# Kernel tuning notes

Measured on AMD Instinct MI355X. Metric: run time of the kernel, lower is better.

Reference implementation:

```python
import jax, jax.numpy as jnp
import numpy as np

B, NELEC, NATOMS, SH_PER_ATOM, NORB, NCTR = 512, 100, 20, 30, 300, 2
NBAS = NATOMS * SH_PER_ATOM  # 600 == NORB * NCTR


def _ipow(x, k):
    # x**k for integer k in {0,1,2}; safe for negative x (cartesian harmonics)
    return jnp.where(k == 0, jnp.ones_like(x), jnp.where(k == 1, x, x * x))


def setup_inputs() -> dict:
    key = jax.random.key(0)
    ks = jax.random.split(key, 7)
    pos = jax.random.normal(ks[0], (B, NELEC * 3), jnp.float32)
    atom_coords = jax.random.normal(ks[1], (NATOMS, 3), jnp.float32)
    bas_exp = jax.random.uniform(ks[2], (NBAS,), jnp.float32, 0.5, 3.0)
    bas_n = jax.random.randint(ks[3], (NBAS,), 0, 3).astype(jnp.float32)
    norm_cst = jax.random.uniform(ks[4], (NBAS,), jnp.float32, 0.5, 1.5)
    bas_coeffs = jax.random.normal(ks[5], (NBAS,), jnp.float32)
    bas_kxyz = jax.random.randint(ks[6], (NBAS, 3), 0, 3)  # kx, ky, kz exponents
    index_ctr = jnp.repeat(jnp.arange(NORB, dtype=jnp.int32), NCTR)  # nbas -> norb
    return {"pos": pos, "atom_coords": atom_coords, "bas_exp": bas_exp,
            "bas_n": bas_n, "norm_cst": norm_cst, "bas_coeffs": bas_coeffs,
            "bas_kxyz": bas_kxyz, "index_ctr": index_ctr}


def reference(pos, atom_coords, bas_exp, bas_n, norm_cst, bas_coeffs, bas_kxyz, index_ctr):
    # gather: per-shell atom coordinates  (NBAS, 3)
    bas_coords = jnp.repeat(atom_coords, SH_PER_ATOM, axis=0)
    # electron - basis-center displacement  (B, Nelec, NBAS, 3)
    xyz = pos.reshape(-1, NELEC, 1, 3) - bas_coords[None, None]
    r2 = jnp.sum(xyz * xyz, axis=-1)                 # (B, Nelec, NBAS)
    r = jnp.sqrt(r2)
    # radial_gaussian: r^n * exp(-alpha r^2)
    R = jnp.power(r, bas_n) * jnp.exp(-bas_exp * r2)
    # cartesian harmonics: x^kx * y^ky * z^kz
    Y = (_ipow(xyz[..., 0], bas_kxyz[:, 0]) *
         _ipow(xyz[..., 1], bas_kxyz[:, 1]) *
         _ipow(xyz[..., 2], bas_kxyz[:, 2]))
    # ao kernel + contraction (segment-sum over basis fns into orbitals)
    vals = (norm_cst * bas_coeffs) * R * Y           # (B, Nelec, NBAS)
    ao = jnp.zeros((pos.shape[0], NELEC, NORB), vals.dtype).at[:, :, index_ctr].add(vals)
    return ao
```

## Files before the change

### kernel.cpp

```cpp
#include <hip/hip_runtime.h>

#define BATCH   512
#define NELEC   100
#define NATOMS  20
#define SH      30
#define NORB    300
#define NBAS    600
#define NROWS   (BATCH * NELEC)
#define GROWS   16
#define NGRP    2
#define ROWS    (GROWS * NGRP)
#define NBLOCKS (NROWS / ROWS)
#define BLOCK   (320 * NGRP)

#define LOG2E 1.4426950408889634f

__global__ __launch_bounds__(BLOCK, 8) void ao_kernel(
    const float* __restrict__ pos,
    const float* __restrict__ atom_coords,
    const float* __restrict__ bas_exp,
    const float* __restrict__ bas_n,
    const float* __restrict__ norm_cst,
    const float* __restrict__ bas_coeffs,
    const int*   __restrict__ bas_kxyz,
    float*       __restrict__ out)
{
    __shared__ float4 spos4[ROWS];

    const int t    = threadIdx.x;
    const int g    = (t >= 320) ? 1 : 0;
    const int tt   = t - 320 * g;
    const int brow = blockIdx.x * ROWS;
    const int row0 = brow + g * GROWS;

    float2 ex2, nn2, nc2, bc2;
    int2 k01, k23, k45;
    float ax = 0.f, ay = 0.f, az = 0.f;
    if (tt < NORB) {
        ex2 = ((const float2*)bas_exp)[tt];
        nn2 = ((const float2*)bas_n)[tt];
        nc2 = ((const float2*)norm_cst)[tt];
        bc2 = ((const float2*)bas_coeffs)[tt];
        k01 = ((const int2*)bas_kxyz)[3 * tt + 0];
        k23 = ((const int2*)bas_kxyz)[3 * tt + 1];
        k45 = ((const int2*)bas_kxyz)[3 * tt + 2];
        const int at = (2 * tt) / SH;
        ax = atom_coords[3 * at + 0];
        ay = atom_coords[3 * at + 1];
        az = atom_coords[3 * at + 2];
    }

    if (t < ROWS * 3) {
        ((float*)spos4)[(t / 3) * 4 + (t % 3)] = pos[(size_t)brow * 3 + t];
    }
    __syncthreads();

    if (tt < NORB) {
        const float c0 = nc2.x * bc2.x;
        const float c1 = nc2.y * bc2.y;
        const float al0 = -ex2.x * LOG2E;
        const float al1 = -ex2.y * LOG2E;
        const int n0 = (int)nn2.x, n1 = (int)nn2.y;
        const float q00 = (n0 == 0) ? c0 : 0.0f, q01 = (n0 == 1) ? c0 : 0.0f, q02 = (n0 == 2) ? c0 : 0.0f;
        const float q10 = (n1 == 0) ? c1 : 0.0f, q11 = (n1 == 1) ? c1 : 0.0f, q12 = (n1 == 2) ? c1 : 0.0f;
        const int kx0 = k01.x, ky0 = k01.y, kz0 = k23.x;
        const int kx1 = k23.y, ky1 = k45.x, kz1 = k45.y;
        const float mx00 = (kx0 == 0), mx01 = (kx0 == 1), mx02 = (kx0 == 2);
        const float my00 = (ky0 == 0), my01 = (ky0 == 1), my02 = (ky0 == 2);
        const float mz00 = (kz0 == 0), mz01 = (kz0 == 1), mz02 = (kz0 == 2);
        const float mx10 = (kx1 == 0), mx11 = (kx1 == 1), mx12 = (kx1 == 2);
        const float my10 = (ky1 == 0), my11 = (ky1 == 1), my12 = (ky1 == 2);
        const float mz10 = (kz1 == 0), mz11 = (kz1 == 1), mz12 = (kz1 == 2);

        float* op = out + (size_t)row0 * NORB + tt;

#pragma unroll 4
        for (int r = 0; r < GROWS; ++r) {
            const float4 p = spos4[g * GROWS + r];

            const float dx = p.x - ax, dy = p.y - ay, dz = p.z - az;
            const float r2 = fmaf(dx, dx, fmaf(dy, dy, dz * dz));
            const float rr = __builtin_amdgcn_sqrtf(r2);

            float e  = __builtin_amdgcn_exp2f(al0 * r2);
            float cR = fmaf(rr, q01, fmaf(r2, q02, q00));
            float yx = fmaf(dx, fmaf(dx, mx02, mx01), mx00);
            float yy = fmaf(dy, fmaf(dy, my02, my01), my00);
            float yz = fmaf(dz, fmaf(dz, mz02, mz01), mz00);
            float v  = (cR * e) * ((yx * yy) * yz);

            e  = __builtin_amdgcn_exp2f(al1 * r2);
            cR = fmaf(rr, q11, fmaf(r2, q12, q10));
            yx = fmaf(dx, fmaf(dx, mx12, mx11), mx10);
            yy = fmaf(dy, fmaf(dy, my12, my11), my10);
            yz = fmaf(dz, fmaf(dz, mz12, mz11), mz10);
            v  = fmaf(cR * e, (yx * yy) * yz, v);

            __builtin_nontemporal_store(v, op);
            op += NORB;
        }
    }
}

extern "C" void kernel_launch(void* const* d_in, const int* in_sizes, int n_in,
                              void* d_out, int out_size, void* d_ws, size_t ws_size,
                              hipStream_t stream) {
    const float* pos         = (const float*)d_in[0];
    const float* atom_coords = (const float*)d_in[1];
    const float* bas_exp     = (const float*)d_in[2];
    const float* bas_n       = (const float*)d_in[3];
    const float* norm_cst    = (const float*)d_in[4];
    const float* bas_coeffs  = (const float*)d_in[5];
    const int*   bas_kxyz    = (const int*)d_in[6];
    float* out = (float*)d_out;

    ao_kernel<<<NBLOCKS, BLOCK, 0, stream>>>(pos, atom_coords, bas_exp, bas_n,
                                             norm_cst, bas_coeffs, bas_kxyz, out);
}
```

Baseline: 102.4 us.

## Use single 320-thread group per block with 32 rows and plain stores

Restructures the block from two 320-thread groups each handling 16 rows into one 320-thread group handling 32 rows, halving block size while keeping the same number of blocks. Each thread now loops over 32 rows, which amortizes the per-thread parameter setup over more work but leaves less parallelism per block. It also replaces nontemporal stores with ordinary stores, changing how the write-dominated output traffic interacts with the cache.

```diff
diff --git a/kernel.cpp b/kernel.cpp
--- a/kernel.cpp
+++ b/kernel.cpp
@@ -7,11 +7,9 @@
 #define NORB    300
 #define NBAS    600
 #define NROWS   (BATCH * NELEC)
-#define GROWS   16
-#define NGRP    2
-#define ROWS    (GROWS * NGRP)
-#define NBLOCKS (NROWS / ROWS)
-#define BLOCK   (320 * NGRP)
+#define GROWS   32
+#define NBLOCKS (NROWS / GROWS)
+#define BLOCK   320
 
 #define LOG2E 1.4426950408889634f
 
@@ -25,37 +23,34 @@
     const int*   __restrict__ bas_kxyz,
     float*       __restrict__ out)
 {
-    __shared__ float4 spos4[ROWS];
+    __shared__ float4 spos4[GROWS];
 
     const int t    = threadIdx.x;
-    const int g    = (t >= 320) ? 1 : 0;
-    const int tt   = t - 320 * g;
-    const int brow = blockIdx.x * ROWS;
-    const int row0 = brow + g * GROWS;
+    const int row0 = blockIdx.x * GROWS;
 
     float2 ex2, nn2, nc2, bc2;
     int2 k01, k23, k45;
     float ax = 0.f, ay = 0.f, az = 0.f;
-    if (tt < NORB) {
-        ex2 = ((const float2*)bas_exp)[tt];
-        nn2 = ((const float2*)bas_n)[tt];
-        nc2 = ((const float2*)norm_cst)[tt];
-        bc2 = ((const float2*)bas_coeffs)[tt];
-        k01 = ((const int2*)bas_kxyz)[3 * tt + 0];
-        k23 = ((const int2*)bas_kxyz)[3 * tt + 1];
-        k45 = ((const int2*)bas_kxyz)[3 * tt + 2];
-        const int at = (2 * tt) / SH;
+    if (t < NORB) {
+        ex2 = ((const float2*)bas_exp)[t];
+        nn2 = ((const float2*)bas_n)[t];
+        nc2 = ((const float2*)norm_cst)[t];
+        bc2 = ((const float2*)bas_coeffs)[t];
+        k01 = ((const int2*)bas_kxyz)[3 * t + 0];
+        k23 = ((const int2*)bas_kxyz)[3 * t + 1];
+        k45 = ((const int2*)bas_kxyz)[3 * t + 2];
+        const int at = (2 * t) / SH;
         ax = atom_coords[3 * at + 0];
         ay = atom_coords[3 * at + 1];
         az = atom_coords[3 * at + 2];
     }
 
-    if (t < ROWS * 3) {
-        ((float*)spos4)[(t / 3) * 4 + (t % 3)] = pos[(size_t)brow * 3 + t];
+    if (t < GROWS * 3) {
+        ((float*)spos4)[(t / 3) * 4 + (t % 3)] = pos[(size_t)row0 * 3 + t];
     }
     __syncthreads();
 
-    if (tt < NORB) {
+    if (t < NORB) {
         const float c0 = nc2.x * bc2.x;
         const float c1 = nc2.y * bc2.y;
         const float al0 = -ex2.x * LOG2E;
@@ -72,11 +67,11 @@
         const float my10 = (ky1 == 0), my11 = (ky1 == 1), my12 = (ky1 == 2);
         const float mz10 = (kz1 == 0), mz11 = (kz1 == 1), mz12 = (kz1 == 2);
 
-        float* op = out + (size_t)row0 * NORB + tt;
+        float* op = out + (size_t)row0 * NORB + t;
 
 #pragma unroll 4
         for (int r = 0; r < GROWS; ++r) {
-            const float4 p = spos4[g * GROWS + r];
+            const float4 p = spos4[r];
 
             const float dx = p.x - ax, dy = p.y - ay, dz = p.z - az;
             const float r2 = fmaf(dx, dx, fmaf(dy, dy, dz * dz));
@@ -96,7 +91,7 @@
             yz = fmaf(dz, fmaf(dz, mz12, mz11), mz10);
             v  = fmaf(cR * e, (yx * yy) * yz, v);
 
-            __builtin_nontemporal_store(v, op);
+            *op = v;
             op += NORB;
         }
     }
```

Measured after the change: 102.1 us. No clear change (-0.3%).
